# Performance work log

Measured on AMD Instinct MI355X. Metric: run time of the kernel, lower is better.

Reference implementation:

```python
import jax, jax.numpy as jnp
import numpy as np

VOCAB = 32000
ROUTE_BIAS = 10.0  # weight on the deterministic one-hot route vs mu logits


def setup_inputs() -> dict:
    key = jax.random.key(0)
    k1, k2, k3, k4, k5, k6 = jax.random.split(key, 6)
    B, S, H = 2, 4096, 1024
    E, Ie = 8, 512  # intermediate_size=4096 -> expert_intermediate=512, fused dim=2*Ie=1024
    return {
        "hidden_states": jax.random.normal(k1, (B, S, H), dtype=jnp.float32),
        "token_ids": jax.random.randint(k2, (B, S), 0, VOCAB),
        "mu": jax.random.normal(k3, (B, S, H), dtype=jnp.float32),
        "gate_up_proj": jax.random.normal(k4, (E, H, 2 * Ie), dtype=jnp.float32) * 0.02,
        "down_proj": jax.random.normal(k5, (E, Ie, H), dtype=jnp.float32) * 0.02,
        "mu_router_w": jax.random.normal(k6, (E, H), dtype=jnp.float32) * 0.02,
    }


def reference(hidden_states, token_ids, mu, gate_up_proj, down_proj, mu_router_w):
    B, S, H = hidden_states.shape
    E, _, F2 = gate_up_proj.shape
    Ie = F2 // 2
    N = B * S

    # deterministic token->expert routing, optionally perturbed by mu logits
    token_to_expert = jnp.arange(VOCAB, dtype=jnp.int32) % E
    base_expert = token_to_expert[jnp.clip(token_ids, 0, VOCAB - 1)]      # [B,S]
    mu_logits = jnp.einsum('bsh,eh->bse', mu, mu_router_w)                 # [B,S,E]
    combined = jax.nn.one_hot(base_expert, E, dtype=mu_logits.dtype) * ROUTE_BIAS + mu_logits
    expert_ids = jnp.argmax(combined, axis=-1).reshape(N)                  # [N]

    x = hidden_states.reshape(N, H)
    tok = jnp.arange(N)

    # compute per-expert GEMM then select per-token expert output
    # (same math as gathering the full weight slab per token, without the
    #  N*H*2Ie gathered-weight blowup of the original torch code)
    gu_all = jnp.einsum('nh,ehf->enf', x, gate_up_proj)                    # [E,N,2Ie]
    gu = gu_all[expert_ids, tok]                                           # [N,2Ie]
    gate, up = gu[:, :Ie], gu[:, Ie:]
    inter = jax.nn.silu(gate) * up                                         # [N,Ie]

    z_all = jnp.einsum('ni,eih->enh', inter, down_proj)                    # [E,N,H]
    out = z_all[expert_ids, tok].reshape(B, S, H)
    return out
```

## Files before the change

kernel.cpp:

```cpp
#include <hip/hip_runtime.h>
#include <hip/hip_bf16.h>
#include <stdint.h>

typedef __bf16 bf16x8 __attribute__((ext_vector_type(8)));
typedef float f32x4 __attribute__((ext_vector_type(4)));

#define ROUTE_BIAS_F 10.0f
#define VOCAB_SZ 32000

__device__ __forceinline__ unsigned short f2bf(float f) {
    union { float f; unsigned u; } v; v.f = f;
    unsigned u = v.u;
    unsigned r = u + 0x7FFFu + ((u >> 16) & 1u);
    return (unsigned short)(r >> 16);
}
__device__ __forceinline__ void ld16(const unsigned short* g, unsigned short* l) {
    __builtin_amdgcn_global_load_lds(
        (const __attribute__((address_space(1))) void*)g,
        (__attribute__((address_space(3))) void*)l, 16, 0, 0);
}

__global__ void k_prep(const float* __restrict__ hidden, const float* __restrict__ mu,
                       const int* __restrict__ tok_ids, const float* __restrict__ rw,
                       unsigned short* __restrict__ xb, int* __restrict__ eids,
                       int H, int N) {
    int lane = threadIdx.x & 63;
    int wv   = threadIdx.x >> 6;
    int tok  = blockIdx.x * 4 + wv;
    if (tok >= N) return;
    const float4* hp = (const float4*)(hidden + (size_t)tok * H);
    const float4* mp = (const float4*)(mu + (size_t)tok * H);
    const float4* rp = (const float4*)rw;
    ushort4* xp = (ushort4*)(xb + (size_t)tok * H);
    int H4 = H >> 2;
    float acc[8];
#pragma unroll
    for (int e = 0; e < 8; ++e) acc[e] = 0.f;
#pragma unroll
    for (int j = 0; j < 4; ++j) {
        int idx = lane + 64 * j;
        float4 h4 = hp[idx];
        ushort4 o;
        o.x = f2bf(h4.x); o.y = f2bf(h4.y); o.z = f2bf(h4.z); o.w = f2bf(h4.w);
        xp[idx] = o;
        float4 m4 = mp[idx];
#pragma unroll
        for (int e = 0; e < 8; ++e) {
            float4 w4 = rp[e * H4 + idx];
            acc[e] += m4.x * w4.x + m4.y * w4.y + m4.z * w4.z + m4.w * w4.w;
        }
    }
#pragma unroll
    for (int e = 0; e < 8; ++e) {
        float v = acc[e];
#pragma unroll
        for (int off = 32; off > 0; off >>= 1) v += __shfl_xor(v, off);
        acc[e] = v;
    }
    if (lane == 0) {
        int t = tok_ids[tok];
        if (t < 0) t = 0;
        if (t > VOCAB_SZ - 1) t = VOCAB_SZ - 1;
        int be = t % 8;
        float best = -1e30f; int bi = 0;
#pragma unroll
        for (int e = 0; e < 8; ++e) {
            float v = acc[e] + (e == be ? ROUTE_BIAS_F : 0.f);
            if (v > best) { best = v; bi = e; }
        }
        eids[tok] = bi;
    }
}

__global__ __launch_bounds__(256) void k_transpose_all(
        const float* __restrict__ gup, const float* __restrict__ dnp,
        unsigned short* __restrict__ wgut, unsigned short* __restrict__ wdnt,
        int H, int F2, int Ie) {
    __shared__ float tile[64][65];
    int z = blockIdx.z;
    const float* inp; unsigned short* outp; int R, C;
    if (z < 8) { R = H; C = F2; inp = gup + (size_t)z * R * C;       outp = wgut + (size_t)z * R * C; }
    else       { R = Ie; C = H; inp = dnp + (size_t)(z - 8) * R * C; outp = wdnt + (size_t)(z - 8) * R * C; }
    int c0 = blockIdx.x * 64, r0 = blockIdx.y * 64;
    if (r0 >= R) return;
    int tid = threadIdx.x;
    int tr = tid >> 4;
    int tc = (tid & 15) * 4;
#pragma unroll
    for (int p = 0; p < 4; ++p) {
        float4 v = *(const float4*)&inp[(size_t)(r0 + tr + 16 * p) * C + c0 + tc];
        tile[tr + 16 * p][tc + 0] = v.x;
        tile[tr + 16 * p][tc + 1] = v.y;
        tile[tr + 16 * p][tc + 2] = v.z;
        tile[tr + 16 * p][tc + 3] = v.w;
    }
    __syncthreads();
#pragma unroll
    for (int p = 0; p < 4; ++p) {
        int c = tr + 16 * p;
        ushort4 o;
        o.x = f2bf(tile[tc + 0][c]);
        o.y = f2bf(tile[tc + 1][c]);
        o.z = f2bf(tile[tc + 2][c]);
        o.w = f2bf(tile[tc + 3][c]);
        *(ushort4*)&outp[(size_t)(c0 + c) * R + r0 + tc] = o;
    }
}

__global__ void k_count(const int* __restrict__ eids,
                        int* __restrict__ blockcnt, int N) {
    __shared__ int cnt[8];
    int tid = threadIdx.x;
    if (tid < 8) cnt[tid] = 0;
    __syncthreads();
    int tok = blockIdx.x * 256 + tid;
    int lane = tid & 63;
    int eid = (tok < N) ? eids[tok] : -1;
#pragma unroll
    for (int e = 0; e < 8; ++e) {
        unsigned long long m = __ballot(eid == e);
        if (lane == 0 && m) atomicAdd(&cnt[e], __popcll(m));
    }
    __syncthreads();
    if (tid < 8) blockcnt[blockIdx.x * 8 + tid] = cnt[tid];
}

__global__ void k_scan(const int* __restrict__ blockcnt,
                       int* __restrict__ counts, int* __restrict__ base_,
                       int* __restrict__ offs, int NB) {
    __shared__ int tot[8];
    int lane = threadIdx.x;
    int e = lane >> 3, g = lane & 7;
    int v[4];
    int s = 0;
#pragma unroll
    for (int i = 0; i < 4; ++i) { v[i] = s; s += blockcnt[(g * 4 + i) * 8 + e]; }
    int inc = s;
#pragma unroll
    for (int d = 1; d < 8; d <<= 1) {
        int t = __shfl_up(inc, d);
        if (g >= d) inc += t;
    }
    int excl = inc - s;
#pragma unroll
    for (int i = 0; i < 4; ++i) offs[(g * 4 + i) * 8 + e] = excl + v[i];
    if (g == 7) { counts[e] = inc; tot[e] = inc; }
    __syncthreads();
    if (lane == 0) {
        int s2 = 0;
#pragma unroll
        for (int i = 0; i < 8; ++i) { base_[i] = s2; s2 += tot[i]; }
    }
}

__global__ void k_scatter(const int* __restrict__ eids,
                          const int* __restrict__ offs,
                          int* __restrict__ list, int N) {
    __shared__ int wavecnt[4][8];
    int tid = threadIdx.x;
    int lane = tid & 63, wv = tid >> 6;
    int tok = blockIdx.x * 256 + tid;
    int eid = (tok < N) ? eids[tok] : -1;
    unsigned long long below = (1ull << lane) - 1ull;
    int myrank = 0;
#pragma unroll
    for (int e = 0; e < 8; ++e) {
        unsigned long long m = __ballot(eid == e);
        if (lane == 0) wavecnt[wv][e] = __popcll(m);
        if (eid == e) myrank = __popcll(m & below);
    }
    __syncthreads();
    if (eid >= 0) {
        int pre = 0;
        for (int w = 0; w < wv; ++w) pre += wavecnt[w][eid];
        int pos = offs[blockIdx.x * 8 + eid] + pre + myrank;
        list[eid * N + pos] = tok;
    }
}

#define TM 128
#define TN 128
#define TK 64

__global__ __launch_bounds__(256, 2) void k_gemm_gateup(
    const unsigned short* __restrict__ X,
    const unsigned short* __restrict__ Wt,
    unsigned short* __restrict__ IT,
    const int* __restrict__ counts, const int* __restrict__ base_,
    const int* __restrict__ list, int N, int H, int Ie) {
    int bid = blockIdx.x;
    int e = bid & 7;
    int t = bid >> 3;
    int nt = t & 7;
    int slot = t >> 3;
    int cnt = counts[e];
    int F2 = 2 * Ie;
    int b = base_[e];
    int nt64 = nt * 64;

    __shared__ __align__(16) unsigned short As[2][TM * TK];
    __shared__ __align__(16) unsigned short Bs[2][TN * TK];

    int tid = threadIdx.x;
    int lane = tid & 63, wv = tid >> 6;
    int wr = (wv >> 1) * 64;
    int wc = (wv & 1) * 64;

    int rowg = lane >> 3;
    int sl   = (lane & 7) ^ rowg;

    const unsigned short* bg[4];
#pragma unroll
    for (int i = 0; i < 4; ++i) {
        int r = wv * 32 + i * 8 + rowg;
        int wrow = (r & 1) * Ie + nt64 + (r >> 1);
        bg[i] = Wt + ((size_t)e * F2 + wrow) * H + sl * 8;
    }

    int q = lane >> 4, m = lane & 15;
    int sw = m & 7;
    int nk = H / TK;

    for (int mt = slot; mt * TM < cnt; mt += 8) {
        int m0 = mt * TM;

        const unsigned short* ag[4];
#pragma unroll
        for (int i = 0; i < 4; ++i) {
            int r = wv * 32 + i * 8 + rowg;
            int gr = m0 + r;
            int tokrow = (gr < cnt) ? list[e * N + gr] : 0;
            ag[i] = X + (size_t)tokrow * H + sl * 8;
        }

        f32x4 acc[4][4];
#pragma unroll
        for (int i = 0; i < 4; ++i)
#pragma unroll
            for (int j = 0; j < 4; ++j) acc[i][j] = (f32x4)(0.f);

#pragma unroll
        for (int i = 0; i < 4; ++i) ld16(ag[i],      &As[0][(wv * 32 + i * 8) * TK]);
#pragma unroll
        for (int i = 0; i < 4; ++i) ld16(bg[i],      &Bs[0][(wv * 32 + i * 8) * TK]);
#pragma unroll
        for (int i = 0; i < 4; ++i) ld16(ag[i] + TK, &As[1][(wv * 32 + i * 8) * TK]);
#pragma unroll
        for (int i = 0; i < 4; ++i) ld16(bg[i] + TK, &Bs[1][(wv * 32 + i * 8) * TK]);

        for (int t_ = 0; t_ < nk; ++t_) {
            asm volatile("s_waitcnt vmcnt(8)" ::: "memory");
            __builtin_amdgcn_s_barrier();

            const unsigned short* Ac = As[t_ & 1];
            const unsigned short* Bc = Bs[t_ & 1];
            bf16x8 af[2][4], bfr[2][4];
#pragma unroll
            for (int s = 0; s < 2; ++s) {
                int ck = (((s * 4) + q) ^ sw) << 3;
#pragma unroll
                for (int im = 0; im < 4; ++im)
                    af[s][im] = *(const bf16x8*)&Ac[(wr + m + im * 16) * TK + ck];
#pragma unroll
                for (int in_ = 0; in_ < 4; ++in_)
                    bfr[s][in_] = *(const bf16x8*)&Bc[(wc + m + in_ * 16) * TK + ck];
            }
            asm volatile("s_waitcnt lgkmcnt(0)" ::: "memory");
            __builtin_amdgcn_s_barrier();

            int tn = t_ + 2; if (tn > nk - 1) tn = nk - 1;
            int kk = tn * TK;
#pragma unroll
            for (int i = 0; i < 4; ++i) ld16(ag[i] + kk, &As[t_ & 1][(wv * 32 + i * 8) * TK]);
#pragma unroll
            for (int i = 0; i < 4; ++i) ld16(bg[i] + kk, &Bs[t_ & 1][(wv * 32 + i * 8) * TK]);

            __builtin_amdgcn_s_setprio(1);
#pragma unroll
            for (int s = 0; s < 2; ++s)
#pragma unroll
                for (int im = 0; im < 4; ++im)
#pragma unroll
                    for (int in_ = 0; in_ < 4; ++in_)
                        acc[im][in_] = __builtin_amdgcn_mfma_f32_16x16x32_bf16(
                            af[s][im], bfr[s][in_], acc[im][in_], 0, 0, 0);
            __builtin_amdgcn_s_setprio(0);
        }
        asm volatile("s_waitcnt vmcnt(0)" ::: "memory");
        __builtin_amdgcn_s_barrier();

#pragma unroll
        for (int im = 0; im < 4; ++im) {
#pragma unroll
            for (int j = 0; j < 4; ++j) {
                int row = wr + im * 16 + q * 4 + j;
                int gr = m0 + row;
#pragma unroll
                for (int in_ = 0; in_ < 4; ++in_) {
                    float v = acc[im][in_][j];
                    float u = __shfl_xor(v, 1);
                    float g = v;
                    float s = g / (1.f + __expf(-g));
                    float res = s * u;
                    if (!(lane & 1) && gr < cnt) {
                        int oc = nt64 + ((wc + in_ * 16 + m) >> 1);
                        IT[(size_t)(b + gr) * Ie + oc] = f2bf(res);
                    }
                }
            }
        }
    }
}

__global__ __launch_bounds__(256, 2) void k_gemm_down(
    const unsigned short* __restrict__ IT,
    const unsigned short* __restrict__ Wt,
    float* __restrict__ OUT,
    const int* __restrict__ counts, const int* __restrict__ base_,
    const int* __restrict__ list, int N, int Ie, int H) {
    int bid = blockIdx.x;
    int e = bid & 7;
    int t = bid >> 3;
    int nt = t & 7;
    int slot = t >> 3;
    int cnt = counts[e];
    int n0 = nt * TN;
    int b = base_[e];

    __shared__ __align__(16) unsigned short As[2][TM * TK];
    __shared__ __align__(16) unsigned short Bs[2][TN * TK];

    int tid = threadIdx.x;
    int lane = tid & 63, wv = tid >> 6;
    int wr = (wv >> 1) * 64;
    int wc = (wv & 1) * 64;

    int rowg = lane >> 3;
    int sl   = (lane & 7) ^ rowg;

    const unsigned short* We = Wt + ((size_t)e * H + n0) * Ie;
    const unsigned short* bg[4];
#pragma unroll
    for (int i = 0; i < 4; ++i) {
        int r = wv * 32 + i * 8 + rowg;
        bg[i] = We + (size_t)r * Ie + sl * 8;
    }

    int q = lane >> 4, m = lane & 15;
    int sw = m & 7;
    int nk = Ie / TK;

    for (int mt = slot; mt * TM < cnt; mt += 8) {
        int m0 = mt * TM;

        const unsigned short* ag[4];
#pragma unroll
        for (int i = 0; i < 4; ++i) {
            int r = wv * 32 + i * 8 + rowg;
            int gr = m0 + r;
            int arow = (gr < cnt) ? (b + gr) : b;
            ag[i] = IT + (size_t)arow * Ie + sl * 8;
        }

        f32x4 acc[4][4];
#pragma unroll
        for (int i = 0; i < 4; ++i)
#pragma unroll
            for (int j = 0; j < 4; ++j) acc[i][j] = (f32x4)(0.f);

#pragma unroll
        for (int i = 0; i < 4; ++i) ld16(ag[i],      &As[0][(wv * 32 + i * 8) * TK]);
#pragma unroll
        for (int i = 0; i < 4; ++i) ld16(bg[i],      &Bs[0][(wv * 32 + i * 8) * TK]);
#pragma unroll
        for (int i = 0; i < 4; ++i) ld16(ag[i] + TK, &As[1][(wv * 32 + i * 8) * TK]);
#pragma unroll
        for (int i = 0; i < 4; ++i) ld16(bg[i] + TK, &Bs[1][(wv * 32 + i * 8) * TK]);

        for (int t_ = 0; t_ < nk; ++t_) {
            asm volatile("s_waitcnt vmcnt(8)" ::: "memory");
            __builtin_amdgcn_s_barrier();

            const unsigned short* Ac = As[t_ & 1];
            const unsigned short* Bc = Bs[t_ & 1];
            bf16x8 af[2][4], bfr[2][4];
#pragma unroll
            for (int s = 0; s < 2; ++s) {
                int ck = (((s * 4) + q) ^ sw) << 3;
#pragma unroll
                for (int im = 0; im < 4; ++im)
                    af[s][im] = *(const bf16x8*)&Ac[(wr + m + im * 16) * TK + ck];
#pragma unroll
                for (int in_ = 0; in_ < 4; ++in_)
                    bfr[s][in_] = *(const bf16x8*)&Bc[(wc + m + in_ * 16) * TK + ck];
            }
            asm volatile("s_waitcnt lgkmcnt(0)" ::: "memory");
            __builtin_amdgcn_s_barrier();

            int tn = t_ + 2; if (tn > nk - 1) tn = nk - 1;
            int kk = tn * TK;
#pragma unroll
            for (int i = 0; i < 4; ++i) ld16(ag[i] + kk, &As[t_ & 1][(wv * 32 + i * 8) * TK]);
#pragma unroll
            for (int i = 0; i < 4; ++i) ld16(bg[i] + kk, &Bs[t_ & 1][(wv * 32 + i * 8) * TK]);

            __builtin_amdgcn_s_setprio(1);
#pragma unroll
            for (int s = 0; s < 2; ++s)
#pragma unroll
                for (int im = 0; im < 4; ++im)
#pragma unroll
                    for (int in_ = 0; in_ < 4; ++in_)
                        acc[im][in_] = __builtin_amdgcn_mfma_f32_16x16x32_bf16(
                            af[s][im], bfr[s][in_], acc[im][in_], 0, 0, 0);
            __builtin_amdgcn_s_setprio(0);
        }
        asm volatile("s_waitcnt vmcnt(0)" ::: "memory");
        __builtin_amdgcn_s_barrier();

#pragma unroll
        for (int im = 0; im < 4; ++im) {
#pragma unroll
            for (int j = 0; j < 4; ++j) {
                int row = wr + im * 16 + q * 4 + j;
                int gr = m0 + row;
                if (gr < cnt) {
                    int tok = list[e * N + gr];
                    float* orow = OUT + (size_t)tok * H + n0;
#pragma unroll
                    for (int in_ = 0; in_ < 4; ++in_) {
                        int col = wc + in_ * 16 + m;
                        orow[col] = acc[im][in_][j];
                    }
                }
            }
        }
    }
}

extern "C" void kernel_launch(void* const* d_in, const int* in_sizes, int n_in,
                              void* d_out, int out_size, void* d_ws, size_t ws_size,
                              hipStream_t stream) {
    const float* hidden   = (const float*)d_in[0];
    const int*   tok_ids  = (const int*)d_in[1];
    const float* mu       = (const float*)d_in[2];
    const float* gup      = (const float*)d_in[3];
    const float* dnp      = (const float*)d_in[4];
    const float* rw       = (const float*)d_in[5];
    float* out = (float*)d_out;

    int N  = in_sizes[1];
    int H  = in_sizes[0] / N;
    int E  = in_sizes[5] / H;
    int F2 = in_sizes[3] / (E * H);
    int Ie = F2 / 2;

    int NB = (N + 255) / 256;

    char* ws = (char*)d_ws;
    size_t o = 0;
    auto alloc = [&](size_t sz) {
        size_t r = o;
        o += (sz + 255) & ~(size_t)255;
        return r;
    };
    int* counts   = (int*)(ws + alloc((size_t)E * 4));
    int* base_    = (int*)(ws + alloc((size_t)E * 4));
    int* eids     = (int*)(ws + alloc((size_t)N * 4));
    int* blockcnt = (int*)(ws + alloc((size_t)NB * 8 * 4));
    int* offs     = (int*)(ws + alloc((size_t)NB * 8 * 4));
    int* list     = (int*)(ws + alloc((size_t)E * N * 4));
    unsigned short* xb   = (unsigned short*)(ws + alloc((size_t)N * H * 2));
    unsigned short* wgut = (unsigned short*)(ws + alloc((size_t)E * F2 * H * 2));
    unsigned short* wdnt = (unsigned short*)(ws + alloc((size_t)E * H * Ie * 2));
    unsigned short* it   = (unsigned short*)(ws + alloc((size_t)N * Ie * 2));

    k_prep<<<dim3((N + 3) / 4), dim3(256), 0, stream>>>(hidden, mu, tok_ids, rw, xb, eids, H, N);

    k_transpose_all<<<dim3(16, 16, 16), dim3(256), 0, stream>>>(gup, dnp, wgut, wdnt, H, F2, Ie);

    k_count<<<dim3(NB), dim3(256), 0, stream>>>(eids, blockcnt, N);
    k_scan<<<dim3(1), dim3(64), 0, stream>>>(blockcnt, counts, base_, offs, NB);
    k_scatter<<<dim3(NB), dim3(256), 0, stream>>>(eids, offs, list, N);

    k_gemm_gateup<<<dim3(E * (Ie / 64) * 8), dim3(256), 0, stream>>>(
        xb, wgut, it, counts, base_, list, N, H, Ie);

    k_gemm_down<<<dim3(E * (H / TN) * 8), dim3(256), 0, stream>>>(
        it, wdnt, out, counts, base_, list, N, Ie, H);
}
```

Measured before the change: 229.1 us.

## Fuse prep and weight transpose kernels, replace count/scan/scatter with atomic scatter

Merges the token prep/routing kernel and the weight transpose-to-bf16 kernel into a single launch partitioned by block index. The separate count, scan and scatter kernels become one atomic-based scatter plus a tiny base scan, with a memset to zero the counters. The transpose stores are widened to 8-element vectors. The aim is fewer launches and less serialization between small kernels. Token order within each expert list is now nondeterministic because of the atomics, though the output values are unaffected.

```diff
diff --git a/kernel.cpp b/kernel.cpp
--- a/kernel.cpp
+++ b/kernel.cpp
@@ -4,6 +4,7 @@
 
 typedef __bf16 bf16x8 __attribute__((ext_vector_type(8)));
 typedef float f32x4 __attribute__((ext_vector_type(4)));
+typedef unsigned short u16x8 __attribute__((ext_vector_type(8)));
 
 #define ROUTE_BIAS_F 10.0f
 #define VOCAB_SZ 32000
@@ -20,161 +21,134 @@
         (__attribute__((address_space(3))) void*)l, 16, 0, 0);
 }
 
-__global__ void k_prep(const float* __restrict__ hidden, const float* __restrict__ mu,
-                       const int* __restrict__ tok_ids, const float* __restrict__ rw,
-                       unsigned short* __restrict__ xb, int* __restrict__ eids,
-                       int H, int N) {
-    int lane = threadIdx.x & 63;
-    int wv   = threadIdx.x >> 6;
-    int tok  = blockIdx.x * 4 + wv;
-    if (tok >= N) return;
-    const float4* hp = (const float4*)(hidden + (size_t)tok * H);
-    const float4* mp = (const float4*)(mu + (size_t)tok * H);
-    const float4* rp = (const float4*)rw;
-    ushort4* xp = (ushort4*)(xb + (size_t)tok * H);
-    int H4 = H >> 2;
-    float acc[8];
-#pragma unroll
-    for (int e = 0; e < 8; ++e) acc[e] = 0.f;
-#pragma unroll
-    for (int j = 0; j < 4; ++j) {
-        int idx = lane + 64 * j;
-        float4 h4 = hp[idx];
-        ushort4 o;
-        o.x = f2bf(h4.x); o.y = f2bf(h4.y); o.z = f2bf(h4.z); o.w = f2bf(h4.w);
-        xp[idx] = o;
-        float4 m4 = mp[idx];
+__global__ __launch_bounds__(256) void k_prep_all(
+        const float* __restrict__ hidden, const float* __restrict__ mu,
+        const int* __restrict__ tok_ids, const float* __restrict__ rw,
+        const float* __restrict__ gup, const float* __restrict__ dnp,
+        unsigned short* __restrict__ xb, int* __restrict__ eids,
+        unsigned short* __restrict__ wgut, unsigned short* __restrict__ wdnt,
+        int H, int N, int F2, int Ie, int NPREP) {
+    __shared__ float tile[64][65];
+    int bid = blockIdx.x;
+    int tid = threadIdx.x;
+
+    if (bid < NPREP) {
+        int lane = tid & 63;
+        int wv   = tid >> 6;
+        int tok  = bid * 4 + wv;
+        if (tok >= N) return;
+        const float4* hp = (const float4*)(hidden + (size_t)tok * H);
+        const float4* mp = (const float4*)(mu + (size_t)tok * H);
+        const float4* rp = (const float4*)rw;
+        ushort4* xp = (ushort4*)(xb + (size_t)tok * H);
+        int H4 = H >> 2;
+        float acc[8];
+#pragma unroll
+        for (int e = 0; e < 8; ++e) acc[e] = 0.f;
+#pragma unroll
+        for (int j = 0; j < 4; ++j) {
+            int idx = lane + 64 * j;
+            float4 h4 = hp[idx];
+            ushort4 o;
+            o.x = f2bf(h4.x); o.y = f2bf(h4.y); o.z = f2bf(h4.z); o.w = f2bf(h4.w);
+            xp[idx] = o;
+            float4 m4 = mp[idx];
+#pragma unroll
+            for (int e = 0; e < 8; ++e) {
+                float4 w4 = rp[e * H4 + idx];
+                acc[e] += m4.x * w4.x + m4.y * w4.y + m4.z * w4.z + m4.w * w4.w;
+            }
+        }
 #pragma unroll
         for (int e = 0; e < 8; ++e) {
-            float4 w4 = rp[e * H4 + idx];
-            acc[e] += m4.x * w4.x + m4.y * w4.y + m4.z * w4.z + m4.w * w4.w;
-        }
-    }
-#pragma unroll
-    for (int e = 0; e < 8; ++e) {
-        float v = acc[e];
-#pragma unroll
-        for (int off = 32; off > 0; off >>= 1) v += __shfl_xor(v, off);
-        acc[e] = v;
-    }
-    if (lane == 0) {
-        int t = tok_ids[tok];
-        if (t < 0) t = 0;
-        if (t > VOCAB_SZ - 1) t = VOCAB_SZ - 1;
-        int be = t % 8;
-        float best = -1e30f; int bi = 0;
-#pragma unroll
-        for (int e = 0; e < 8; ++e) {
-            float v = acc[e] + (e == be ? ROUTE_BIAS_F : 0.f);
-            if (v > best) { best = v; bi = e; }
-        }
-        eids[tok] = bi;
-    }
-}
-
-__global__ __launch_bounds__(256) void k_transpose_all(
-        const float* __restrict__ gup, const float* __restrict__ dnp,
-        unsigned short* __restrict__ wgut, unsigned short* __restrict__ wdnt,
-        int H, int F2, int Ie) {
-    __shared__ float tile[64][65];
-    int z = blockIdx.z;
-    const float* inp; unsigned short* outp; int R, C;
-    if (z < 8) { R = H; C = F2; inp = gup + (size_t)z * R * C;       outp = wgut + (size_t)z * R * C; }
-    else       { R = Ie; C = H; inp = dnp + (size_t)(z - 8) * R * C; outp = wdnt + (size_t)(z - 8) * R * C; }
-    int c0 = blockIdx.x * 64, r0 = blockIdx.y * 64;
-    if (r0 >= R) return;
+            float v = acc[e];
+#pragma unroll
+            for (int off = 32; off > 0; off >>= 1) v += __shfl_xor(v, off);
+            acc[e] = v;
+        }
+        if (lane == 0) {
+            int t = tok_ids[tok];
+            if (t < 0) t = 0;
+            if (t > VOCAB_SZ - 1) t = VOCAB_SZ - 1;
+            int be = t % 8;
+            float best = -1e30f; int bi = 0;
+#pragma unroll
+            for (int e = 0; e < 8; ++e) {
+                float v = acc[e] + (e == be ? ROUTE_BIAS_F : 0.f);
+                if (v > best) { best = v; bi = e; }
+            }
+            eids[tok] = bi;
+        }
+        return;
+    }
+
+    int tb = bid - NPREP;
+    const float* inp; unsigned short* outp; int R, C, c0, r0;
+    if (tb < 2048) {
+        int z = tb >> 8, t = tb & 255;
+        R = H; C = F2;
+        inp  = gup  + (size_t)z * R * C;
+        outp = wgut + (size_t)z * R * C;
+        c0 = (t & 15) * 64; r0 = (t >> 4) * 64;
+    } else {
+        int tb2 = tb - 2048;
+        int z = tb2 >> 7, t = tb2 & 127;
+        R = Ie; C = H;
+        inp  = dnp  + (size_t)z * R * C;
+        outp = wdnt + (size_t)z * R * C;
+        c0 = (t & 15) * 64; r0 = (t >> 4) * 64;
+    }
+    {
+        int tr = tid >> 4;
+        int tc = (tid & 15) * 4;
+#pragma unroll
+        for (int p = 0; p < 4; ++p) {
+            float4 v = *(const float4*)&inp[(size_t)(r0 + tr + 16 * p) * C + c0 + tc];
+            tile[tr + 16 * p][tc + 0] = v.x;
+            tile[tr + 16 * p][tc + 1] = v.y;
+            tile[tr + 16 * p][tc + 2] = v.z;
+            tile[tr + 16 * p][tc + 3] = v.w;
+        }
+        __syncthreads();
+        int tr2 = tid >> 3;
+        int tc2 = (tid & 7) * 8;
+#pragma unroll
+        for (int p = 0; p < 2; ++p) {
+            int c = tr2 + 32 * p;
+            u16x8 o;
+#pragma unroll
+            for (int j = 0; j < 8; ++j) o[j] = f2bf(tile[tc2 + j][c]);
+            *(u16x8*)&outp[(size_t)(c0 + c) * R + r0 + tc2] = o;
+        }
+    }
+}
+
+__global__ void k_scatter(const int* __restrict__ eids,
+                          int* __restrict__ cnt8,
+                          int* __restrict__ list, int N) {
     int tid = threadIdx.x;
-    int tr = tid >> 4;
-    int tc = (tid & 15) * 4;
-#pragma unroll
-    for (int p = 0; p < 4; ++p) {
-        float4 v = *(const float4*)&inp[(size_t)(r0 + tr + 16 * p) * C + c0 + tc];
-        tile[tr + 16 * p][tc + 0] = v.x;
-        tile[tr + 16 * p][tc + 1] = v.y;
-        tile[tr + 16 * p][tc + 2] = v.z;
-        tile[tr + 16 * p][tc + 3] = v.w;
-    }
-    __syncthreads();
-#pragma unroll
-    for (int p = 0; p < 4; ++p) {
-        int c = tr + 16 * p;
-        ushort4 o;
-        o.x = f2bf(tile[tc + 0][c]);
-        o.y = f2bf(tile[tc + 1][c]);
-        o.z = f2bf(tile[tc + 2][c]);
-        o.w = f2bf(tile[tc + 3][c]);
-        *(ushort4*)&outp[(size_t)(c0 + c) * R + r0 + tc] = o;
-    }
-}
-
-__global__ void k_count(const int* __restrict__ eids,
-                        int* __restrict__ blockcnt, int N) {
-    __shared__ int cnt[8];
-    int tid = threadIdx.x;
-    if (tid < 8) cnt[tid] = 0;
-    __syncthreads();
-    int tok = blockIdx.x * 256 + tid;
     int lane = tid & 63;
-    int eid = (tok < N) ? eids[tok] : -1;
-#pragma unroll
-    for (int e = 0; e < 8; ++e) {
-        unsigned long long m = __ballot(eid == e);
-        if (lane == 0 && m) atomicAdd(&cnt[e], __popcll(m));
-    }
-    __syncthreads();
-    if (tid < 8) blockcnt[blockIdx.x * 8 + tid] = cnt[tid];
-}
-
-__global__ void k_scan(const int* __restrict__ blockcnt,
-                       int* __restrict__ counts, int* __restrict__ base_,
-                       int* __restrict__ offs, int NB) {
-    __shared__ int tot[8];
-    int lane = threadIdx.x;
-    int e = lane >> 3, g = lane & 7;
-    int v[4];
-    int s = 0;
-#pragma unroll
-    for (int i = 0; i < 4; ++i) { v[i] = s; s += blockcnt[(g * 4 + i) * 8 + e]; }
-    int inc = s;
-#pragma unroll
-    for (int d = 1; d < 8; d <<= 1) {
-        int t = __shfl_up(inc, d);
-        if (g >= d) inc += t;
-    }
-    int excl = inc - s;
-#pragma unroll
-    for (int i = 0; i < 4; ++i) offs[(g * 4 + i) * 8 + e] = excl + v[i];
-    if (g == 7) { counts[e] = inc; tot[e] = inc; }
-    __syncthreads();
-    if (lane == 0) {
-        int s2 = 0;
-#pragma unroll
-        for (int i = 0; i < 8; ++i) { base_[i] = s2; s2 += tot[i]; }
-    }
-}
-
-__global__ void k_scatter(const int* __restrict__ eids,
-                          const int* __restrict__ offs,
-                          int* __restrict__ list, int N) {
-    __shared__ int wavecnt[4][8];
-    int tid = threadIdx.x;
-    int lane = tid & 63, wv = tid >> 6;
     int tok = blockIdx.x * 256 + tid;
     int eid = (tok < N) ? eids[tok] : -1;
     unsigned long long below = (1ull << lane) - 1ull;
-    int myrank = 0;
 #pragma unroll
     for (int e = 0; e < 8; ++e) {
         unsigned long long m = __ballot(eid == e);
-        if (lane == 0) wavecnt[wv][e] = __popcll(m);
-        if (eid == e) myrank = __popcll(m & below);
-    }
-    __syncthreads();
-    if (eid >= 0) {
-        int pre = 0;
-        for (int w = 0; w < wv; ++w) pre += wavecnt[w][eid];
-        int pos = offs[blockIdx.x * 8 + eid] + pre + myrank;
-        list[eid * N + pos] = tok;
+        int old = 0;
+        if (lane == 0 && m) old = atomicAdd(&cnt8[e], __popcll(m));
+        old = __shfl(old, 0);
+        if (eid == e) {
+            int pos = old + __popcll(m & below);
+            list[e * N + pos] = tok;
+        }
+    }
+}
+
+__global__ void k_scan_base(const int* __restrict__ cnt8, int* __restrict__ base_) {
+    if (threadIdx.x == 0) {
+        int s = 0;
+#pragma unroll
+        for (int i = 0; i < 8; ++i) { base_[i] = s; s += cnt8[i]; }
     }
 }
 
@@ -455,8 +429,6 @@
     int F2 = in_sizes[3] / (E * H);
     int Ie = F2 / 2;
 
-    int NB = (N + 255) / 256;
-
     char* ws = (char*)d_ws;
     size_t o = 0;
     auto alloc = [&](size_t sz) {
@@ -464,28 +436,29 @@
         o += (sz + 255) & ~(size_t)255;
         return r;
     };
-    int* counts   = (int*)(ws + alloc((size_t)E * 4));
+    int* cnt8     = (int*)(ws + alloc((size_t)E * 4));
     int* base_    = (int*)(ws + alloc((size_t)E * 4));
     int* eids     = (int*)(ws + alloc((size_t)N * 4));
-    int* blockcnt = (int*)(ws + alloc((size_t)NB * 8 * 4));
-    int* offs     = (int*)(ws + alloc((size_t)NB * 8 * 4));
     int* list     = (int*)(ws + alloc((size_t)E * N * 4));
     unsigned short* xb   = (unsigned short*)(ws + alloc((size_t)N * H * 2));
     unsigned short* wgut = (unsigned short*)(ws + alloc((size_t)E * F2 * H * 2));
     unsigned short* wdnt = (unsigned short*)(ws + alloc((size_t)E * H * Ie * 2));
     unsigned short* it   = (unsigned short*)(ws + alloc((size_t)N * Ie * 2));
 
-    k_prep<<<dim3((N + 3) / 4), dim3(256), 0, stream>>>(hidden, mu, tok_ids, rw, xb, eids, H, N);
-
-    k_transpose_all<<<dim3(16, 16, 16), dim3(256), 0, stream>>>(gup, dnp, wgut, wdnt, H, F2, Ie);
-
-    k_count<<<dim3(NB), dim3(256), 0, stream>>>(eids, blockcnt, N);
-    k_scan<<<dim3(1), dim3(64), 0, stream>>>(blockcnt, counts, base_, offs, NB);
-    k_scatter<<<dim3(NB), dim3(256), 0, stream>>>(eids, offs, list, N);
+    hipMemsetAsync(cnt8, 0, (size_t)E * 4, stream);
+
+    int NPREP = (N + 3) / 4;
+    int NTRANS = 2048 + 1024;
+    k_prep_all<<<dim3(NPREP + NTRANS), dim3(256), 0, stream>>>(
+        hidden, mu, tok_ids, rw, gup, dnp, xb, eids, wgut, wdnt, H, N, F2, Ie, NPREP);
+
+    int NB = (N + 255) / 256;
+    k_scatter<<<dim3(NB), dim3(256), 0, stream>>>(eids, cnt8, list, N);
+    k_scan_base<<<dim3(1), dim3(64), 0, stream>>>(cnt8, base_);
 
     k_gemm_gateup<<<dim3(E * (Ie / 64) * 8), dim3(256), 0, stream>>>(
-        xb, wgut, it, counts, base_, list, N, H, Ie);
+        xb, wgut, it, cnt8, base_, list, N, H, Ie);
 
     k_gemm_down<<<dim3(E * (H / TN) * 8), dim3(256), 0, stream>>>(
-        it, wdnt, out, counts, base_, list, N, Ie, H);
-}
+        it, wdnt, out, cnt8, base_, list, N, Ie, H);
+}
```

New measurement: 236.8 us. +3.4%, slower.
